# Performance work log

Measured on AMD Instinct MI355X. Metric: run time of the kernel, lower is better.

The kernel has to match this reference:

```python
import jax, jax.numpy as jnp
import numpy as np

B, T, D = 4, 1024, 1024
NEXP, TOPK = 8, 2
N = B * T
# eval capacity: floor(TOPK * 2.0 * N / NEXP) = 2048, already even and >= min_capacity
CAP = 2048
LN_EPS = 1e-5


def setup_inputs() -> dict:
    key = jax.random.key(0)
    ks = jax.random.split(key, 4)
    x = jax.random.normal(ks[0], (B, T, D), jnp.float32)
    w_g = jax.random.normal(ks[1], (D, NEXP), jnp.float32) * 0.02
    c_fc = jax.random.normal(ks[2], (NEXP, D, 4 * D), jnp.float32) * 0.02
    c_proj = jax.random.normal(ks[3], (NEXP, 4 * D, D), jnp.float32) * 0.02
    ln_w = jnp.ones((D,), jnp.float32)
    ln_b = jnp.zeros((D,), jnp.float32)
    return {"x": x, "w_g": w_g, "c_fc": c_fc, "c_proj": c_proj, "ln_w": ln_w, "ln_b": ln_b}


def moe_forward(x, w_g, c_fc, c_proj, ln_w, ln_b):
    xf = x.reshape(N, D)
    # --- Router ---
    logits = xf @ w_g                                   # [N, E]
    topk_vals, topk_idx = jax.lax.top_k(logits, TOPK)   # [N, K]
    masked = jnp.full_like(logits, -jnp.inf)
    masked = masked.at[jnp.arange(N)[:, None], topk_idx].set(topk_vals)
    probs = jax.nn.softmax(masked, axis=-1)             # [N, E]

    # capacity-based ranking (slot 0 for all tokens first, then slot 1, ...)
    onehot = jax.nn.one_hot(topk_idx, NEXP, dtype=jnp.int32)     # [N, K, E]
    exp_mask = jnp.transpose(onehot, (1, 0, 2))                  # [K, N, E]
    rank = jnp.cumsum(exp_mask.reshape(TOPK * N, NEXP), axis=0) - 1
    rank = rank.reshape(TOPK, N, NEXP)
    exp_mask = exp_mask * (rank < CAP).astype(jnp.int32)         # drop overflow
    rank_tok = jnp.sum(exp_mask * rank, axis=-1)                 # [K, N]
    exp_w = exp_mask.astype(probs.dtype) * probs[None]           # [K, N, E]
    rank_oh = jax.nn.one_hot(rank_tok, CAP, dtype=probs.dtype)   # [K, N, C]
    cb_weight = jnp.einsum('kne,knc->nec', exp_w, rank_oh)       # [N, E, C]
    sec_mask = (cb_weight != 0).astype(x.dtype)                  # dispatch mask

    # --- dispatch -> experts -> combine ---
    xb = jnp.einsum('nec,nd->ecd', sec_mask, xf)                 # [E, C, D]
    h = jax.nn.gelu(jnp.einsum('ecd,edf->ecf', xb, c_fc), approximate=False)
    eo = jnp.einsum('ecf,efd->ecd', h, c_proj)                   # [E, C, D]
    out = jnp.einsum('nec,ecd->nd', cb_weight, eo)               # [N, D]

    # --- LayerNorm ---
    mu = out.mean(-1, keepdims=True)
    var = out.var(-1, keepdims=True)
    out = (out - mu) / jnp.sqrt(var + LN_EPS) * ln_w + ln_b
    return out.reshape(B, T, D)


def reference(x, w_g, c_fc, c_proj, ln_w, ln_b):
    return moe_forward(x, w_g, c_fc, c_proj, ln_w, ln_b)
```

## Files before the change

kernel.cpp:

```cpp
#include <hip/hip_runtime.h>
#include <math.h>

#define NEXP 8
#define CAP 2048
#define NTOK 4096
#define DDIM 1024
#define FDIM 4096

typedef __bf16 bf16x8 __attribute__((ext_vector_type(8)));
typedef float f32x4 __attribute__((ext_vector_type(4)));
typedef unsigned short u16x8 __attribute__((ext_vector_type(8)));

__device__ __forceinline__ unsigned short f2bf(float f) {
    unsigned int u = __float_as_uint(f);
    u += 0x7FFFu + ((u >> 16) & 1u);
    return (unsigned short)(u >> 16);
}
__device__ __forceinline__ float bf2f(unsigned short h) {
    return __uint_as_float(((unsigned int)h) << 16);
}

__device__ __forceinline__ void gld_lds16(const void* g, void* l) {
    __builtin_amdgcn_global_load_lds((const __attribute__((address_space(1))) void*)g,
                                     (__attribute__((address_space(3))) void*)l, 16, 0, 0);
}

__global__ __launch_bounds__(256) void transpose_cvt64(const float* __restrict__ in,
                                                       unsigned short* __restrict__ out,
                                                       int R, int C) {
    __shared__ float tile[64][65];
    int e = blockIdx.z;
    const float* ip = in + (size_t)e * R * C;
    unsigned short* op = out + (size_t)e * R * C;
    int c0 = blockIdx.x * 64, r0 = blockIdx.y * 64;
    int t = threadIdx.x;
#pragma unroll
    for (int i = 0; i < 4; i++) {
        int rr = i * 16 + (t >> 4);
        int cc = (t & 15) * 4;
        float4 v = *(const float4*)&ip[(size_t)(r0 + rr) * C + c0 + cc];
        tile[rr][cc] = v.x; tile[rr][cc + 1] = v.y; tile[rr][cc + 2] = v.z; tile[rr][cc + 3] = v.w;
    }
    __syncthreads();
    int c = t >> 2, rb = (t & 3) * 16;
    u16x8 o0, o1;
#pragma unroll
    for (int j = 0; j < 8; j++) o0[j] = f2bf(tile[rb + j][c]);
#pragma unroll
    for (int j = 0; j < 8; j++) o1[j] = f2bf(tile[rb + 8 + j][c]);
    unsigned short* dst = op + (size_t)(c0 + c) * R + r0 + rb;
    *(u16x8*)dst = o0;
    *(u16x8*)(dst + 8) = o1;
}

__global__ __launch_bounds__(256) void router_kernel(const float* __restrict__ x,
                                                     const float* __restrict__ wg,
                                                     int2* __restrict__ e01,
                                                     float2* __restrict__ p01) {
    int wid = threadIdx.x >> 6, lane = threadIdx.x & 63;
    int n = blockIdx.x * 4 + wid;
    float acc[8];
#pragma unroll
    for (int i = 0; i < 8; i++) acc[i] = 0.f;
    const float4* xr = (const float4*)(x + (size_t)n * DDIM);
#pragma unroll
    for (int j = 0; j < 4; j++) {
        float4 xv = xr[j * 64 + lane];
        int base = (j * 64 + lane) * 4;
        float xs[4] = {xv.x, xv.y, xv.z, xv.w};
#pragma unroll
        for (int t = 0; t < 4; t++) {
            const float4* wr = (const float4*)(wg + (size_t)(base + t) * 8);
            float4 w0 = wr[0], w1 = wr[1];
            acc[0] += xs[t] * w0.x; acc[1] += xs[t] * w0.y;
            acc[2] += xs[t] * w0.z; acc[3] += xs[t] * w0.w;
            acc[4] += xs[t] * w1.x; acc[5] += xs[t] * w1.y;
            acc[6] += xs[t] * w1.z; acc[7] += xs[t] * w1.w;
        }
    }
#pragma unroll
    for (int off = 32; off > 0; off >>= 1) {
#pragma unroll
        for (int i = 0; i < 8; i++) acc[i] += __shfl_xor(acc[i], off);
    }
    if (lane == 0) {
        int i0 = 0; float v0 = acc[0];
#pragma unroll
        for (int q = 1; q < 8; q++) { if (acc[q] > v0) { v0 = acc[q]; i0 = q; } }
        int i1 = -1; float v1 = -3.0e38f;
#pragma unroll
        for (int q = 0; q < 8; q++) { if (q != i0 && acc[q] > v1) { v1 = acc[q]; i1 = q; } }
        float ea = expf(v0 - v0), eb = expf(v1 - v0);
        float inv = 1.f / (ea + eb);
        e01[n] = make_int2(i0, i1);
        p01[n] = make_float2(ea * inv, eb * inv);
    }
}

__global__ void assign_kernel(const int2* __restrict__ e01, int* __restrict__ counts,
                              int* __restrict__ assign_row, int* __restrict__ tok_slot) {
    int lane = threadIdx.x;
    int base[8];
#pragma unroll
    for (int i = 0; i < 8; i++) base[i] = 0;
    unsigned long long below = ((unsigned long long)1 << lane) - 1ull;
    int2 cur = e01[lane];
    for (int pass = 0; pass < 2; ++pass) {
        for (int t = 0; t < NTOK; t += 64) {
            int n = t + lane;
            int2 nxt;
            if (t + 64 < NTOK) nxt = e01[t + 64 + lane];
            else nxt = (pass == 0) ? e01[lane] : make_int2(0, 0);
            int ex = (pass == 0) ? cur.x : cur.y;
            int slot = -1;
#pragma unroll
            for (int q = 0; q < 8; q++) {
                unsigned long long m = __ballot(ex == q);
                if (ex == q) slot = base[q] + __popcll(m & below);
                base[q] += __popcll(m);
            }
            if (slot < CAP) {
                assign_row[ex * CAP + slot] = n;
                tok_slot[2 * n + pass] = slot;
            } else {
                tok_slot[2 * n + pass] = -1;
            }
            cur = nxt;
        }
    }
    if (lane < 8) counts[lane] = base[lane] > CAP ? CAP : base[lane];
}

__global__ __launch_bounds__(256) void gather_rows(const float* __restrict__ x,
                                                   const int* __restrict__ assign_row,
                                                   const int* __restrict__ counts,
                                                   unsigned short* __restrict__ xg) {
    int e = blockIdx.y;
    int wid = threadIdx.x >> 6, lane = threadIdx.x & 63;
    int slot = blockIdx.x * 4 + wid;
    if (slot >= counts[e]) return;
    int n = assign_row[e * CAP + slot];
    const float4* src = (const float4*)(x + (size_t)n * DDIM);
    unsigned short* dst = xg + ((size_t)e * CAP + slot) * DDIM;
#pragma unroll
    for (int j = 0; j < 4; j++) {
        float4 v = src[j * 64 + lane];
        ushort4 o;
        o.x = f2bf(v.x); o.y = f2bf(v.y); o.z = f2bf(v.z); o.w = f2bf(v.w);
        *(ushort4*)(dst + (size_t)(j * 64 + lane) * 4) = o;
    }
}

template <bool GELU, int KC>
__global__ __launch_bounds__(512, 2) void gemm_8ph(const unsigned short* __restrict__ A,
                                                   const unsigned short* __restrict__ Bt,
                                                   unsigned short* __restrict__ Cout,
                                                   const int* __restrict__ counts,
                                                   int Ncols, int Ktot) {
    __shared__ __align__(16) char smem[131072];

    int gx = gridDim.x, gy = gridDim.y;
    int nwg = gx * gy * gridDim.z;
    int flat = blockIdx.x + gx * (blockIdx.y + gy * blockIdx.z);
    int cpx = nwg >> 3;
    int swz = (flat & 7) * cpx + (flat >> 3);
    int gxy = gx * gy;
    int zz = swz / gxy;
    int r2 = swz - zz * gxy;
    int by = r2 / gx;
    int bx = r2 - by * gx;
    int e = zz / KC, kc = zz % KC;

    int cnt = counts[e];
    int row0 = by * 256;
    if (row0 >= cnt) return;
    int col0 = bx * 256;
    const int Ksub = Ktot / KC;
    const int NT = Ksub >> 6;

    const unsigned short* Ab = A + ((size_t)e * CAP + row0) * Ktot + (size_t)kc * Ksub;
    const unsigned short* Bb = Bt + ((size_t)e * Ncols + col0) * Ktot + (size_t)kc * Ksub;

    int tid = threadIdx.x, w = tid >> 6, lane = tid & 63;
    int wm = w >> 2, wn = w & 3;

    int kel = (((tid & 3) ^ ((tid >> 3) & 3)) * 8);

    int aoff[8], boff[4];
    int c0 = lane >> 4;
#pragma unroll
    for (int mq = 0; mq < 8; mq++) {
        int row = wm * 128 + mq * 16 + (lane & 15);
        aoff[mq] = row * 64 + ((c0 ^ ((row >> 1) & 3)) << 4);
    }
#pragma unroll
    for (int nq = 0; nq < 4; nq++) {
        int row = wn * 64 + nq * 16 + (lane & 15);
        boff[nq] = row * 64 + ((c0 ^ ((row >> 1) & 3)) << 4);
    }

    auto stage_half = [&](int hidx) {
        int tau = hidx >> 2, h = hidx & 3;
        const unsigned short* src = (h & 1) ? Bb : Ab;
        char* base = smem + ((h & 1) ? 65536 : 0) + (((tau & 1) << 1) + (h >> 1)) * 16384;
        size_t kq = (size_t)tau * 64 + ((h >> 1) << 5) + kel;
#pragma unroll
        for (int i = 0; i < 2; i++)
            gld_lds16(src + (size_t)(i * 128 + (tid >> 2)) * Ktot + kq,
                      base + i * 8192 + tid * 16);
    };

    f32x4 acc[8][4] = {};

#pragma unroll
    for (int hh = 0; hh < 6; ++hh) stage_half(hh);
    asm volatile("s_waitcnt vmcnt(4)" ::: "memory");
    __builtin_amdgcn_sched_barrier(0);
    __builtin_amdgcn_s_barrier();

    const int H = 4 * NT;
    for (int t = 0; t < NT; ++t) {
        const int db = t & 1;
        const char* A0 = smem + (db * 2 + 0) * 16384;
        const char* A1 = smem + (db * 2 + 1) * 16384;
        const char* B0 = smem + 65536 + (db * 2 + 0) * 16384;
        const char* B1 = smem + 65536 + (db * 2 + 1) * 16384;
        const int h6 = 4 * t + 6;
        bf16x8 a[4], b[4];

#pragma unroll
        for (int n = 0; n < 4; n++) b[n] = *(const bf16x8*)(B0 + boff[n]);
#pragma unroll
        for (int m = 0; m < 4; m++) a[m] = *(const bf16x8*)(A0 + aoff[m]);
        if (h6 + 0 < H) stage_half(h6 + 0);
        __builtin_amdgcn_sched_barrier(0);
        __builtin_amdgcn_s_barrier();
        asm volatile("s_waitcnt lgkmcnt(0)" ::: "memory");
        __builtin_amdgcn_sched_barrier(0);
        __builtin_amdgcn_s_setprio(1);
#pragma unroll
        for (int m = 0; m < 4; m++)
#pragma unroll
            for (int n = 0; n < 4; n++)
                acc[m][n] = __builtin_amdgcn_mfma_f32_16x16x32_bf16(a[m], b[n], acc[m][n], 0, 0, 0);
        __builtin_amdgcn_s_setprio(0);
        __builtin_amdgcn_s_barrier();

#pragma unroll
        for (int m = 0; m < 4; m++) a[m] = *(const bf16x8*)(A0 + aoff[4 + m]);
        if (h6 + 1 < H) stage_half(h6 + 1);
        __builtin_amdgcn_sched_barrier(0);
        __builtin_amdgcn_s_barrier();
        asm volatile("s_waitcnt lgkmcnt(0)" ::: "memory");
        __builtin_amdgcn_sched_barrier(0);
        __builtin_amdgcn_s_setprio(1);
#pragma unroll
        for (int m = 0; m < 4; m++)
#pragma unroll
            for (int n = 0; n < 4; n++)
                acc[4 + m][n] = __builtin_amdgcn_mfma_f32_16x16x32_bf16(a[m], b[n], acc[4 + m][n], 0, 0, 0);
        __builtin_amdgcn_s_setprio(0);
        __builtin_amdgcn_s_barrier();

#pragma unroll
        for (int n = 0; n < 4; n++) b[n] = *(const bf16x8*)(B1 + boff[n]);
#pragma unroll
        for (int m = 0; m < 4; m++) a[m] = *(const bf16x8*)(A1 + aoff[m]);
        if (h6 + 2 < H) stage_half(h6 + 2);
        __builtin_amdgcn_sched_barrier(0);
        __builtin_amdgcn_s_barrier();
        asm volatile("s_waitcnt lgkmcnt(0)" ::: "memory");
        __builtin_amdgcn_sched_barrier(0);
        __builtin_amdgcn_s_setprio(1);
#pragma unroll
        for (int m = 0; m < 4; m++)
#pragma unroll
            for (int n = 0; n < 4; n++)
                acc[m][n] = __builtin_amdgcn_mfma_f32_16x16x32_bf16(a[m], b[n], acc[m][n], 0, 0, 0);
        __builtin_amdgcn_s_setprio(0);
        __builtin_amdgcn_s_barrier();

#pragma unroll
        for (int m = 0; m < 4; m++) a[m] = *(const bf16x8*)(A1 + aoff[4 + m]);
        if (h6 + 3 < H) stage_half(h6 + 3);
        if (t + 2 < NT)      asm volatile("s_waitcnt vmcnt(4)" ::: "memory");
        else if (t + 1 < NT) asm volatile("s_waitcnt vmcnt(0)" ::: "memory");
        __builtin_amdgcn_sched_barrier(0);
        __builtin_amdgcn_s_barrier();
        asm volatile("s_waitcnt lgkmcnt(0)" ::: "memory");
        __builtin_amdgcn_sched_barrier(0);
        __builtin_amdgcn_s_setprio(1);
#pragma unroll
        for (int m = 0; m < 4; m++)
#pragma unroll
            for (int n = 0; n < 4; n++)
                acc[4 + m][n] = __builtin_amdgcn_mfma_f32_16x16x32_bf16(a[m], b[n], acc[4 + m][n], 0, 0, 0);
        __builtin_amdgcn_s_setprio(0);
        __builtin_amdgcn_s_barrier();
    }

    unsigned short* Cb = Cout + (((size_t)(kc * NEXP + e) * CAP + row0)) * Ncols + col0;
#pragma unroll
    for (int mq = 0; mq < 8; mq++)
#pragma unroll
        for (int n = 0; n < 4; n++)
#pragma unroll
            for (int j = 0; j < 4; j++) {
                int lr = wm * 128 + mq * 16 + ((lane >> 4) << 2) + j;
                int lc = wn * 64 + n * 16 + (lane & 15);
                float v = acc[mq][n][j];
                if constexpr (GELU) {
                    float g = 0.5f * v * (1.0f + erff(v * 0.70710678118654752f));
                    Cb[(size_t)lr * Ncols + lc] = f2bf(g);
                } else {
                    Cb[(size_t)lr * Ncols + lc] = f2bf(v);
                }
            }
}

__global__ __launch_bounds__(256) void combine_ln_kernel(const unsigned short* __restrict__ pb,
                                                         const int2* __restrict__ e01,
                                                         const float2* __restrict__ p01,
                                                         const int* __restrict__ tok_slot,
                                                         const float* __restrict__ lnw,
                                                         const float* __restrict__ lnb,
                                                         float* __restrict__ out) {
    const size_t PLANE = (size_t)NEXP * CAP * DDIM;
    int n = blockIdx.x, t = threadIdx.x;
    int2 e = e01[n];
    float2 p = p01[n];
    int s0 = tok_slot[2 * n], s1 = tok_slot[2 * n + 1];
    float o0 = 0.f, o1 = 0.f, o2 = 0.f, o3 = 0.f;
    if (s0 >= 0) {
        size_t base = ((size_t)e.x * CAP + s0) * DDIM;
        ushort4 u0 = ((const ushort4*)(pb + base))[t];
        ushort4 u1 = ((const ushort4*)(pb + PLANE + base))[t];
        o0 += p.x * (bf2f(u0.x) + bf2f(u1.x));
        o1 += p.x * (bf2f(u0.y) + bf2f(u1.y));
        o2 += p.x * (bf2f(u0.z) + bf2f(u1.z));
        o3 += p.x * (bf2f(u0.w) + bf2f(u1.w));
    }
    if (s1 >= 0) {
        size_t base = ((size_t)e.y * CAP + s1) * DDIM;
        ushort4 u0 = ((const ushort4*)(pb + base))[t];
        ushort4 u1 = ((const ushort4*)(pb + PLANE + base))[t];
        o0 += p.y * (bf2f(u0.x) + bf2f(u1.x));
        o1 += p.y * (bf2f(u0.y) + bf2f(u1.y));
        o2 += p.y * (bf2f(u0.z) + bf2f(u1.z));
        o3 += p.y * (bf2f(u0.w) + bf2f(u1.w));
    }
    float s = o0 + o1 + o2 + o3;
    float sq = o0 * o0 + o1 * o1 + o2 * o2 + o3 * o3;
#pragma unroll
    for (int off = 32; off > 0; off >>= 1) {
        s += __shfl_xor(s, off);
        sq += __shfl_xor(sq, off);
    }
    __shared__ float red[8];
    int wid = t >> 6, lane = t & 63;
    if (lane == 0) { red[wid] = s; red[4 + wid] = sq; }
    __syncthreads();
    s = red[0] + red[1] + red[2] + red[3];
    sq = red[4] + red[5] + red[6] + red[7];
    float mu = s * (1.f / DDIM);
    float var = sq * (1.f / DDIM) - mu * mu;
    float inv = rsqrtf(var + 1e-5f);
    const float4 w = ((const float4*)lnw)[t];
    const float4 b = ((const float4*)lnb)[t];
    float4 r;
    r.x = (o0 - mu) * inv * w.x + b.x;
    r.y = (o1 - mu) * inv * w.y + b.y;
    r.z = (o2 - mu) * inv * w.z + b.z;
    r.w = (o3 - mu) * inv * w.w + b.w;
    ((float4*)(out + (size_t)n * DDIM))[t] = r;
}

extern "C" void kernel_launch(void* const* d_in, const int* in_sizes, int n_in,
                              void* d_out, int out_size, void* d_ws, size_t ws_size,
                              hipStream_t stream) {
    const float* x   = (const float*)d_in[0];
    const float* wg  = (const float*)d_in[1];
    const float* cfc = (const float*)d_in[2];
    const float* cpr = (const float*)d_in[3];
    const float* lnw = (const float*)d_in[4];
    const float* lnb = (const float*)d_in[5];
    float* out = (float*)d_out;

    char* ws = (char*)d_ws;
    size_t off = 0;
    auto take = [&](size_t b) {
        char* p = ws + off;
        off += (b + 255) & ~(size_t)255;
        return p;
    };
    unsigned short* cfct = (unsigned short*)take((size_t)NEXP * FDIM * DDIM * 2);
    unsigned short* pb = cfct;
    unsigned short* cprt = (unsigned short*)take((size_t)NEXP * DDIM * FDIM * 2);
    unsigned short* xg   = (unsigned short*)take((size_t)NEXP * CAP * DDIM * 2);
    unsigned short* h    = (unsigned short*)take((size_t)NEXP * CAP * FDIM * 2);
    int2*   e01      = (int2*)take(NTOK * sizeof(int2));
    float2* p01      = (float2*)take(NTOK * sizeof(float2));
    int*    tok_slot = (int*)take((size_t)NTOK * 2 * 4);
    int*    assign_row = (int*)take((size_t)NEXP * CAP * 4);
    int*    counts   = (int*)take(256);

    transpose_cvt64<<<dim3(FDIM / 64, DDIM / 64, NEXP), 256, 0, stream>>>(cfc, cfct, DDIM, FDIM);
    transpose_cvt64<<<dim3(DDIM / 64, FDIM / 64, NEXP), 256, 0, stream>>>(cpr, cprt, FDIM, DDIM);
    router_kernel<<<NTOK / 4, 256, 0, stream>>>(x, wg, e01, p01);
    assign_kernel<<<1, 64, 0, stream>>>(e01, counts, assign_row, tok_slot);
    gather_rows<<<dim3(CAP / 4, NEXP), 256, 0, stream>>>(x, assign_row, counts, xg);
    gemm_8ph<true, 1><<<dim3(FDIM / 256, CAP / 256, NEXP), 512, 0, stream>>>(xg, cfct, h, counts, FDIM, DDIM);
    gemm_8ph<false, 2><<<dim3(DDIM / 256, CAP / 256, NEXP * 2), 512, 0, stream>>>(h, cprt, pb, counts, DDIM, FDIM);
    combine_ln_kernel<<<NTOK, 256, 0, stream>>>(pb, e01, p01, tok_slot, lnw, lnb, out);
}
```

Measured before the change: 411.6 us.

## Split expert GEMM into specialized fc/proj kernels with simpler K-32 pipelines

```diff
diff --git a/kernel.cpp b/kernel.cpp
--- a/kernel.cpp
+++ b/kernel.cpp
@@ -151,13 +151,109 @@
     }
 }
 
-template <bool GELU, int KC>
-__global__ __launch_bounds__(512, 2) void gemm_8ph(const unsigned short* __restrict__ A,
-                                                   const unsigned short* __restrict__ Bt,
-                                                   unsigned short* __restrict__ Cout,
-                                                   const int* __restrict__ counts,
-                                                   int Ncols, int Ktot) {
-    __shared__ __align__(16) char smem[131072];
+__global__ __launch_bounds__(512, 2) void gemm_fc(const unsigned short* __restrict__ A,
+                                                  const unsigned short* __restrict__ Bt,
+                                                  unsigned short* __restrict__ H,
+                                                  const int* __restrict__ counts) {
+    constexpr int ABYTES = 16384;
+    constexpr int BUFB = 32768;
+    __shared__ __align__(16) char smem[2 * BUFB];
+
+    int gx = gridDim.x, gy = gridDim.y;
+    int nwg = gx * gy * gridDim.z;
+    int flat = blockIdx.x + gx * (blockIdx.y + gy * blockIdx.z);
+    int cpx = nwg >> 3;
+    int swz = (flat & 7) * cpx + (flat >> 3);
+    int gxy = gx * gy;
+    int e = swz / gxy;
+    int r2 = swz - e * gxy;
+    int by = r2 / gx;
+    int bx = r2 - by * gx;
+
+    int cnt = counts[e];
+    int row0 = by * 256;
+    if (row0 >= cnt) return;
+    int col0 = bx * 256;
+
+    int tid = threadIdx.x, w = tid >> 6, lane = tid & 63;
+    int wm = w >> 2, wn = w & 3;
+
+    const unsigned short* Ab = A + ((size_t)e * CAP + row0) * DDIM;
+    const unsigned short* Bb = Bt + ((size_t)e * FDIM + col0) * DDIM;
+    const int NT = DDIM / 32;
+
+    int kel = (((tid & 3) ^ ((tid >> 3) & 3)) * 8);
+    int aoff[8], boff[4];
+    int c0 = lane >> 4;
+#pragma unroll
+    for (int mq = 0; mq < 8; mq++) {
+        int row = wm * 128 + mq * 16 + (lane & 15);
+        aoff[mq] = row * 64 + ((c0 ^ ((row >> 1) & 3)) << 4);
+    }
+#pragma unroll
+    for (int nq = 0; nq < 4; nq++) {
+        int row = wn * 64 + nq * 16 + (lane & 15);
+        boff[nq] = row * 64 + ((c0 ^ ((row >> 1) & 3)) << 4);
+    }
+
+    auto stage = [&](int tt) {
+        int bb = (tt & 1) * BUFB;
+        size_t kt = (size_t)tt * 32 + kel;
+#pragma unroll
+        for (int i = 0; i < 2; i++)
+            gld_lds16(Ab + (size_t)(i * 128 + (tid >> 2)) * DDIM + kt, smem + bb + i * 8192 + tid * 16);
+#pragma unroll
+        for (int i = 0; i < 2; i++)
+            gld_lds16(Bb + (size_t)(i * 128 + (tid >> 2)) * DDIM + kt, smem + bb + ABYTES + i * 8192 + tid * 16);
+    };
+
+    f32x4 acc[8][4] = {};
+
+    stage(0);
+    __builtin_amdgcn_sched_barrier(0);
+    __syncthreads();
+
+    for (int t = 0; t < NT; ++t) {
+        const int bb = (t & 1) * BUFB;
+        if (t + 1 < NT) stage(t + 1);
+        __builtin_amdgcn_sched_barrier(0);
+        bf16x8 a[8], b[4];
+#pragma unroll
+        for (int mq = 0; mq < 8; mq++) a[mq] = *(const bf16x8*)(smem + bb + aoff[mq]);
+#pragma unroll
+        for (int nq = 0; nq < 4; nq++) b[nq] = *(const bf16x8*)(smem + bb + ABYTES + boff[nq]);
+        __builtin_amdgcn_s_setprio(1);
+#pragma unroll
+        for (int mq = 0; mq < 8; mq++)
+#pragma unroll
+            for (int nq = 0; nq < 4; nq++)
+                acc[mq][nq] = __builtin_amdgcn_mfma_f32_16x16x32_bf16(a[mq], b[nq], acc[mq][nq], 0, 0, 0);
+        __builtin_amdgcn_s_setprio(0);
+        __syncthreads();
+    }
+
+    unsigned short* Cb = H + ((size_t)e * CAP + row0) * FDIM + col0;
+#pragma unroll
+    for (int mq = 0; mq < 8; mq++)
+#pragma unroll
+        for (int nq = 0; nq < 4; nq++)
+#pragma unroll
+            for (int j = 0; j < 4; j++) {
+                int lr = wm * 128 + mq * 16 + ((lane >> 4) << 2) + j;
+                int lc = wn * 64 + nq * 16 + (lane & 15);
+                float v = acc[mq][nq][j];
+                float g = 0.5f * v * (1.0f + erff(v * 0.70710678118654752f));
+                Cb[(size_t)lr * FDIM + lc] = f2bf(g);
+            }
+}
+
+__global__ __launch_bounds__(512, 2) void gemm_pj(const unsigned short* __restrict__ A,
+                                                  const unsigned short* __restrict__ Bt,
+                                                  unsigned short* __restrict__ pb,
+                                                  const int* __restrict__ counts) {
+    constexpr int ABYTES = 16384;
+    constexpr int BUFB = 32768;
+    __shared__ __align__(16) char smem[3 * BUFB];
 
     int gx = gridDim.x, gy = gridDim.y;
     int nwg = gx * gy * gridDim.z;
@@ -169,23 +265,22 @@
     int r2 = swz - zz * gxy;
     int by = r2 / gx;
     int bx = r2 - by * gx;
-    int e = zz / KC, kc = zz % KC;
+    int e = zz >> 1, kc = zz & 1;
 
     int cnt = counts[e];
     int row0 = by * 256;
     if (row0 >= cnt) return;
     int col0 = bx * 256;
-    const int Ksub = Ktot / KC;
-    const int NT = Ksub >> 6;
-
-    const unsigned short* Ab = A + ((size_t)e * CAP + row0) * Ktot + (size_t)kc * Ksub;
-    const unsigned short* Bb = Bt + ((size_t)e * Ncols + col0) * Ktot + (size_t)kc * Ksub;
+    const int Ksub = FDIM / 2;
+    const int NT = Ksub / 32;
 
     int tid = threadIdx.x, w = tid >> 6, lane = tid & 63;
     int wm = w >> 2, wn = w & 3;
 
+    const unsigned short* Ab = A + ((size_t)e * CAP + row0) * FDIM + (size_t)kc * Ksub;
+    const unsigned short* Bb = Bt + ((size_t)e * DDIM + col0) * FDIM + (size_t)kc * Ksub;
+
     int kel = (((tid & 3) ^ ((tid >> 3) & 3)) * 8);
-
     int aoff[8], boff[4];
     int c0 = lane >> 4;
 #pragma unroll
@@ -199,122 +294,56 @@
         boff[nq] = row * 64 + ((c0 ^ ((row >> 1) & 3)) << 4);
     }
 
-    auto stage_half = [&](int hidx) {
-        int tau = hidx >> 2, h = hidx & 3;
-        const unsigned short* src = (h & 1) ? Bb : Ab;
-        char* base = smem + ((h & 1) ? 65536 : 0) + (((tau & 1) << 1) + (h >> 1)) * 16384;
-        size_t kq = (size_t)tau * 64 + ((h >> 1) << 5) + kel;
+    auto stage = [&](int tt) {
+        int bb = (tt % 3) * BUFB;
+        size_t kt = (size_t)tt * 32 + kel;
 #pragma unroll
         for (int i = 0; i < 2; i++)
-            gld_lds16(src + (size_t)(i * 128 + (tid >> 2)) * Ktot + kq,
-                      base + i * 8192 + tid * 16);
+            gld_lds16(Ab + (size_t)(i * 128 + (tid >> 2)) * FDIM + kt, smem + bb + i * 8192 + tid * 16);
+#pragma unroll
+        for (int i = 0; i < 2; i++)
+            gld_lds16(Bb + (size_t)(i * 128 + (tid >> 2)) * FDIM + kt, smem + bb + ABYTES + i * 8192 + tid * 16);
     };
 
     f32x4 acc[8][4] = {};
 
-#pragma unroll
-    for (int hh = 0; hh < 6; ++hh) stage_half(hh);
-    asm volatile("s_waitcnt vmcnt(4)" ::: "memory");
+    stage(0); stage(1);
+    asm volatile("s_waitcnt vmcnt(4) lgkmcnt(0)" ::: "memory");
     __builtin_amdgcn_sched_barrier(0);
     __builtin_amdgcn_s_barrier();
 
-    const int H = 4 * NT;
     for (int t = 0; t < NT; ++t) {
-        const int db = t & 1;
-        const char* A0 = smem + (db * 2 + 0) * 16384;
-        const char* A1 = smem + (db * 2 + 1) * 16384;
-        const char* B0 = smem + 65536 + (db * 2 + 0) * 16384;
-        const char* B1 = smem + 65536 + (db * 2 + 1) * 16384;
-        const int h6 = 4 * t + 6;
-        bf16x8 a[4], b[4];
-
-#pragma unroll
-        for (int n = 0; n < 4; n++) b[n] = *(const bf16x8*)(B0 + boff[n]);
-#pragma unroll
-        for (int m = 0; m < 4; m++) a[m] = *(const bf16x8*)(A0 + aoff[m]);
-        if (h6 + 0 < H) stage_half(h6 + 0);
+        const int bb = (t % 3) * BUFB;
+        if (t + 2 < NT) stage(t + 2);
+        __builtin_amdgcn_sched_barrier(0);
+        bf16x8 a[8], b[4];
+#pragma unroll
+        for (int mq = 0; mq < 8; mq++) a[mq] = *(const bf16x8*)(smem + bb + aoff[mq]);
+#pragma unroll
+        for (int nq = 0; nq < 4; nq++) b[nq] = *(const bf16x8*)(smem + bb + ABYTES + boff[nq]);
+        __builtin_amdgcn_s_setprio(1);
+#pragma unroll
+        for (int mq = 0; mq < 8; mq++)
+#pragma unroll
+            for (int nq = 0; nq < 4; nq++)
+                acc[mq][nq] = __builtin_amdgcn_mfma_f32_16x16x32_bf16(a[mq], b[nq], acc[mq][nq], 0, 0, 0);
+        __builtin_amdgcn_s_setprio(0);
+        if (t + 2 < NT) asm volatile("s_waitcnt vmcnt(4) lgkmcnt(0)" ::: "memory");
+        else            asm volatile("s_waitcnt vmcnt(0) lgkmcnt(0)" ::: "memory");
         __builtin_amdgcn_sched_barrier(0);
         __builtin_amdgcn_s_barrier();
-        asm volatile("s_waitcnt lgkmcnt(0)" ::: "memory");
-        __builtin_amdgcn_sched_barrier(0);
-        __builtin_amdgcn_s_setprio(1);
-#pragma unroll
-        for (int m = 0; m < 4; m++)
-#pragma unroll
-            for (int n = 0; n < 4; n++)
-                acc[m][n] = __builtin_amdgcn_mfma_f32_16x16x32_bf16(a[m], b[n], acc[m][n], 0, 0, 0);
-        __builtin_amdgcn_s_setprio(0);
-        __builtin_amdgcn_s_barrier();
-
-#pragma unroll
-        for (int m = 0; m < 4; m++) a[m] = *(const bf16x8*)(A0 + aoff[4 + m]);
-        if (h6 + 1 < H) stage_half(h6 + 1);
-        __builtin_amdgcn_sched_barrier(0);
-        __builtin_amdgcn_s_barrier();
-        asm volatile("s_waitcnt lgkmcnt(0)" ::: "memory");
-        __builtin_amdgcn_sched_barrier(0);
-        __builtin_amdgcn_s_setprio(1);
-#pragma unroll
-        for (int m = 0; m < 4; m++)
-#pragma unroll
-            for (int n = 0; n < 4; n++)
-                acc[4 + m][n] = __builtin_amdgcn_mfma_f32_16x16x32_bf16(a[m], b[n], acc[4 + m][n], 0, 0, 0);
-        __builtin_amdgcn_s_setprio(0);
-        __builtin_amdgcn_s_barrier();
-
-#pragma unroll
-        for (int n = 0; n < 4; n++) b[n] = *(const bf16x8*)(B1 + boff[n]);
-#pragma unroll
-        for (int m = 0; m < 4; m++) a[m] = *(const bf16x8*)(A1 + aoff[m]);
-        if (h6 + 2 < H) stage_half(h6 + 2);
-        __builtin_amdgcn_sched_barrier(0);
-        __builtin_amdgcn_s_barrier();
-        asm volatile("s_waitcnt lgkmcnt(0)" ::: "memory");
-        __builtin_amdgcn_sched_barrier(0);
-        __builtin_amdgcn_s_setprio(1);
-#pragma unroll
-        for (int m = 0; m < 4; m++)
-#pragma unroll
-            for (int n = 0; n < 4; n++)
-                acc[m][n] = __builtin_amdgcn_mfma_f32_16x16x32_bf16(a[m], b[n], acc[m][n], 0, 0, 0);
-        __builtin_amdgcn_s_setprio(0);
-        __builtin_amdgcn_s_barrier();
-
-#pragma unroll
-        for (int m = 0; m < 4; m++) a[m] = *(const bf16x8*)(A1 + aoff[4 + m]);
-        if (h6 + 3 < H) stage_half(h6 + 3);
-        if (t + 2 < NT)      asm volatile("s_waitcnt vmcnt(4)" ::: "memory");
-        else if (t + 1 < NT) asm volatile("s_waitcnt vmcnt(0)" ::: "memory");
-        __builtin_amdgcn_sched_barrier(0);
-        __builtin_amdgcn_s_barrier();
-        asm volatile("s_waitcnt lgkmcnt(0)" ::: "memory");
-        __builtin_amdgcn_sched_barrier(0);
-        __builtin_amdgcn_s_setprio(1);
-#pragma unroll
-        for (int m = 0; m < 4; m++)
-#pragma unroll
-            for (int n = 0; n < 4; n++)
-                acc[4 + m][n] = __builtin_amdgcn_mfma_f32_16x16x32_bf16(a[m], b[n], acc[4 + m][n], 0, 0, 0);
-        __builtin_amdgcn_s_setprio(0);
-        __builtin_amdgcn_s_barrier();
-    }
-
-    unsigned short* Cb = Cout + (((size_t)(kc * NEXP + e) * CAP + row0)) * Ncols + col0;
+    }
+
+    unsigned short* Cb = pb + (((size_t)(kc * NEXP + e) * CAP + row0)) * DDIM + col0;
 #pragma unroll
     for (int mq = 0; mq < 8; mq++)
 #pragma unroll
-        for (int n = 0; n < 4; n++)
+        for (int nq = 0; nq < 4; nq++)
 #pragma unroll
             for (int j = 0; j < 4; j++) {
                 int lr = wm * 128 + mq * 16 + ((lane >> 4) << 2) + j;
-                int lc = wn * 64 + n * 16 + (lane & 15);
-                float v = acc[mq][n][j];
-                if constexpr (GELU) {
-                    float g = 0.5f * v * (1.0f + erff(v * 0.70710678118654752f));
-                    Cb[(size_t)lr * Ncols + lc] = f2bf(g);
-                } else {
-                    Cb[(size_t)lr * Ncols + lc] = f2bf(v);
-                }
+                int lc = wn * 64 + nq * 16 + (lane & 15);
+                Cb[(size_t)lr * DDIM + lc] = f2bf(acc[mq][nq][j]);
             }
 }
 
@@ -409,7 +438,7 @@
     router_kernel<<<NTOK / 4, 256, 0, stream>>>(x, wg, e01, p01);
     assign_kernel<<<1, 64, 0, stream>>>(e01, counts, assign_row, tok_slot);
     gather_rows<<<dim3(CAP / 4, NEXP), 256, 0, stream>>>(x, assign_row, counts, xg);
-    gemm_8ph<true, 1><<<dim3(FDIM / 256, CAP / 256, NEXP), 512, 0, stream>>>(xg, cfct, h, counts, FDIM, DDIM);
-    gemm_8ph<false, 2><<<dim3(DDIM / 256, CAP / 256, NEXP * 2), 512, 0, stream>>>(h, cprt, pb, counts, DDIM, FDIM);
+    gemm_fc<<<dim3(FDIM / 256, CAP / 256, NEXP), 512, 0, stream>>>(xg, cfct, h, counts);
+    gemm_pj<<<dim3(DDIM / 256, CAP / 256, NEXP * 2), 512, 0, stream>>>(h, cprt, pb, counts);
     combine_ln_kernel<<<NTOK, 256, 0, stream>>>(pb, e01, p01, tok_slot, lnw, lnb, out);
 }
```

Result: no change. 404.1 us (-1.8%).
